# Performance work log

Hardware: AMD Instinct MI355X
Metric: run time of the kernel (lower is better)

## Reference

```python
import jax, jax.numpy as jnp
import numpy as np

T, B, I, H = 128, 256, 512, 1024  # time, batch, input_size, hidden_size


def setup_inputs() -> dict:
    key = jax.random.key(0)
    k1, k2, k3, k4, k5 = jax.random.split(key, 5)
    s = 1.0 / np.sqrt(H)  # matches torch GRUCell uniform(-1/sqrt(H), 1/sqrt(H)) scale
    return {
        "input_seq": jax.random.normal(k1, (T, B, I), dtype=jnp.float32),
        "W_ih": jax.random.uniform(k2, (3 * H, I), minval=-s, maxval=s, dtype=jnp.float32),
        "W_hh": jax.random.uniform(k3, (3 * H, H), minval=-s, maxval=s, dtype=jnp.float32),
        "b_ih": jax.random.uniform(k4, (3 * H,), minval=-s, maxval=s, dtype=jnp.float32),
        "b_hh": jax.random.uniform(k5, (3 * H,), minval=-s, maxval=s, dtype=jnp.float32),
    }


def reference(input_seq, W_ih, W_hh, b_ih, b_hh):
    # Original torch code calls GRUCell(input_seq[i]) with NO hidden state and never
    # feeds the output back, so hx = 0 at EVERY step -> no recurrence; fully vectorizable.
    Hd = W_hh.shape[1]
    # input gates for all timesteps at once: (T, B, 3H)
    gi = jnp.einsum('tbi,gi->tbg', input_seq, W_ih) + b_ih
    # hidden gates with hx = 0: zeros @ W_hh.T + b_hh == b_hh broadcast, shape (B, 3H)
    h0 = jnp.zeros((input_seq.shape[1], Hd), dtype=input_seq.dtype)
    gh = h0 @ W_hh.T + b_hh
    i_r, i_z, i_n = gi[..., :Hd], gi[..., Hd:2 * Hd], gi[..., 2 * Hd:]
    h_r, h_z, h_n = gh[..., :Hd], gh[..., Hd:2 * Hd], gh[..., 2 * Hd:]
    r = jax.nn.sigmoid(i_r + h_r)
    z = jax.nn.sigmoid(i_z + h_z)
    n = jnp.tanh(i_n + r * h_n)
    h = (1.0 - z) * n + z * h0  # z*h0 == 0, kept for faithfulness
    # torch.stack(output, dim=1) -> (B, T, H)
    return jnp.transpose(h, (1, 0, 2))
```

## Files before the change

### kernel.cpp

```cpp
#include <hip/hip_runtime.h>
#include <hip/hip_bf16.h>

using f32x4  = __attribute__((ext_vector_type(4))) float;
using bf16x8 = __attribute__((ext_vector_type(8))) short;
using s16x4  = __attribute__((ext_vector_type(4))) short;

#define TT 128
#define BB 256
#define II 512
#define HH 1024
#define MM (TT * BB)
#define BM 128
#define BH 64
#define BK 64
#define NTHREADS 256

__device__ __forceinline__ short f2bf(float f) {
    unsigned u = __float_as_uint(f);
    u = u + 0x7FFFu + ((u >> 16) & 1u);
    return (short)(u >> 16);
}

__device__ __forceinline__ float sigmoid_f(float x) {
    float e = __expf(-fabsf(x));
    float s = 1.0f / (1.0f + e);
    return x >= 0.0f ? s : 1.0f - s;
}

__device__ __forceinline__ float tanh_f(float x) {
    float e = __expf(-2.0f * fabsf(x));
    float t = (1.0f - e) / (1.0f + e);
    return x >= 0.0f ? t : -t;
}

__device__ __forceinline__ void gload_lds16(const void* g, void* l) {
    __builtin_amdgcn_global_load_lds((const __attribute__((address_space(1))) unsigned*)g,
                                     (__attribute__((address_space(3))) unsigned*)l,
                                     16, 0, 0);
}

__global__ __launch_bounds__(256)
void cvt_bf16_kernel(const float* __restrict__ src, short* __restrict__ dst, int n8) {
    const int stride = gridDim.x * blockDim.x;
    for (int i = blockIdx.x * blockDim.x + threadIdx.x; i < n8; i += stride) {
        f32x4 v0 = ((const f32x4*)src)[2 * i];
        f32x4 v1 = ((const f32x4*)src)[2 * i + 1];
        bf16x8 o;
        o[0] = f2bf(v0.x); o[1] = f2bf(v0.y); o[2] = f2bf(v0.z); o[3] = f2bf(v0.w);
        o[4] = f2bf(v1.x); o[5] = f2bf(v1.y); o[6] = f2bf(v1.z); o[7] = f2bf(v1.w);
        ((bf16x8*)dst)[i] = o;
    }
}

__global__ __launch_bounds__(NTHREADS, 3)
void gru_gemm_kernel(const short* __restrict__ Abf,
                     const short* __restrict__ Wbf,
                     const float* __restrict__ bih,
                     const float* __restrict__ bhh,
                     float* __restrict__ out)
{
    __shared__ short As[BM * BK];
    __shared__ short Ws[3 * BH * BK];

    const int tid  = threadIdx.x;
    const int wid  = tid >> 6;
    const int lane = tid & 63;
    const int l15  = lane & 15;
    const int l4   = lane >> 4;

    const int mtile = blockIdx.x >> 4;
    const int htile = blockIdx.x & 15;
    const int m0 = mtile * BM;
    const int h0 = htile * BH;

    const int lr8 = lane >> 3;
    const int lc  = lane & 7;
    const int csw = (lc * 16) ^ (lr8 << 4);

    f32x4 acc[2][12];
    #pragma unroll
    for (int i = 0; i < 2; ++i)
        #pragma unroll
        for (int j = 0; j < 12; ++j)
            acc[i][j] = (f32x4){0.f, 0.f, 0.f, 0.f};

    const char* Ab = (const char*)Abf;
    const char* Wb = (const char*)Wbf;

    for (int kt = 0; kt < II / BK; ++kt) {
        const int kb = kt * (BK * 2);

        #pragma unroll
        for (int j = 0; j < 4; ++j) {
            const int it  = wid * 4 + j;
            const int row = it * 8 + lr8;
            gload_lds16(Ab + (size_t)(m0 + row) * (II * 2) + kb + csw,
                        (char*)As + it * 1024);
        }
        #pragma unroll
        for (int j = 0; j < 6; ++j) {
            const int iw  = wid * 6 + j;
            const int row = iw * 8 + lr8;
            const int g   = row >> 6;
            const int wr  = row & 63;
            gload_lds16(Wb + (size_t)(g * HH + h0 + wr) * (II * 2) + kb + csw,
                        (char*)Ws + iw * 1024);
        }
        __syncthreads();

        const int xsw = (l15 & 7) << 4;
        #pragma unroll
        for (int kk = 0; kk < 2; ++kk) {
            const int cb = kk * 64 + l4 * 16;
            const int r0 = wid * 32 + l15;
            bf16x8 a0 = *(const bf16x8*)((const char*)As + r0 * 128 + (cb ^ xsw));
            bf16x8 a1 = *(const bf16x8*)((const char*)As + (r0 + 16) * 128 + (cb ^ xsw));
            #pragma unroll
            for (int nf = 0; nf < 12; ++nf) {
                const int rn = nf * 16 + l15;
                bf16x8 b = *(const bf16x8*)((const char*)Ws + rn * 128 + (cb ^ xsw));
                acc[0][nf] = __builtin_amdgcn_mfma_f32_16x16x32_bf16(a0, b, acc[0][nf], 0, 0, 0);
                acc[1][nf] = __builtin_amdgcn_mfma_f32_16x16x32_bf16(a1, b, acc[1][nf], 0, 0, 0);
            }
        }
        __syncthreads();
    }

    #pragma unroll
    for (int nf = 0; nf < 4; ++nf) {
        const int h = h0 + nf * 16 + l15;
        const float bir = bih[h]          + bhh[h];
        const float biz = bih[HH + h]     + bhh[HH + h];
        const float bin = bih[2 * HH + h];
        const float bhn = bhh[2 * HH + h];
        #pragma unroll
        for (int mf = 0; mf < 2; ++mf) {
            const f32x4 ra = acc[mf][nf];
            const f32x4 za = acc[mf][nf + 4];
            const f32x4 na = acc[mf][nf + 8];
            #pragma unroll
            for (int j = 0; j < 4; ++j) {
                const int m = m0 + wid * 32 + mf * 16 + l4 * 4 + j;
                const int t = m >> 8;
                const int b = m & 255;
                const float r = sigmoid_f(ra[j] + bir);
                const float z = sigmoid_f(za[j] + biz);
                const float n = tanh_f(na[j] + bin + r * bhn);
                out[(size_t)b * (TT * HH) + (size_t)t * HH + h] = (1.0f - z) * n;
            }
        }
    }
}

__global__ __launch_bounds__(NTHREADS, 2)
void gru_fused_kernel(const float* __restrict__ A,
                      const float* __restrict__ Wih,
                      const float* __restrict__ bih,
                      const float* __restrict__ bhh,
                      float* __restrict__ out)
{
    __shared__ short As[BM * BK];
    __shared__ short Ws[3 * BH * BK];

    const int tid  = threadIdx.x;
    const int wid  = tid >> 6;
    const int lane = tid & 63;
    const int l15  = lane & 15;
    const int l4   = lane >> 4;

    const int mtile = blockIdx.x >> 4;
    const int htile = blockIdx.x & 15;
    const int m0 = mtile * BM;
    const int h0 = htile * BH;

    const int rbase = tid >> 4;
    const int c4    = tid & 15;
    const int swz   = (rbase & 7) << 3;

    f32x4 acc[2][12];
    #pragma unroll
    for (int i = 0; i < 2; ++i)
        #pragma unroll
        for (int j = 0; j < 12; ++j)
            acc[i][j] = (f32x4){0.f, 0.f, 0.f, 0.f};

    for (int kt = 0; kt < II / BK; ++kt) {
        const int k0 = kt * BK;
        __syncthreads();
        const float* Ab = A + (size_t)(m0 + rbase) * II + k0 + c4 * 4;
        #pragma unroll
        for (int i = 0; i < 8; ++i) {
            f32x4 v = *(const f32x4*)(Ab + (size_t)i * 16 * II);
            s16x4 hv;
            hv.x = f2bf(v.x); hv.y = f2bf(v.y); hv.z = f2bf(v.z); hv.w = f2bf(v.w);
            const int idx = (i * 16 + rbase) * BK + ((c4 * 4) ^ swz);
            *(s16x4*)(As + idx) = hv;
        }
        #pragma unroll
        for (int i = 0; i < 12; ++i) {
            const int row = i * 16 + rbase;
            const int g   = row >> 6;
            const int r   = row & 63;
            f32x4 v = *(const f32x4*)(Wih + (size_t)(g * HH + h0 + r) * II + k0 + c4 * 4);
            s16x4 hv;
            hv.x = f2bf(v.x); hv.y = f2bf(v.y); hv.z = f2bf(v.z); hv.w = f2bf(v.w);
            const int idx = row * BK + ((c4 * 4) ^ swz);
            *(s16x4*)(Ws + idx) = hv;
        }
        __syncthreads();

        #pragma unroll
        for (int kk = 0; kk < 2; ++kk) {
            const int kc = kk * 32 + l4 * 8;
            const int r0 = wid * 32 + l15;
            const int r1 = r0 + 16;
            bf16x8 a0 = *(const bf16x8*)(As + r0 * BK + (kc ^ ((r0 & 7) << 3)));
            bf16x8 a1 = *(const bf16x8*)(As + r1 * BK + (kc ^ ((r1 & 7) << 3)));
            #pragma unroll
            for (int nf = 0; nf < 12; ++nf) {
                const int rn = nf * 16 + l15;
                bf16x8 b = *(const bf16x8*)(Ws + rn * BK + (kc ^ ((rn & 7) << 3)));
                acc[0][nf] = __builtin_amdgcn_mfma_f32_16x16x32_bf16(a0, b, acc[0][nf], 0, 0, 0);
                acc[1][nf] = __builtin_amdgcn_mfma_f32_16x16x32_bf16(a1, b, acc[1][nf], 0, 0, 0);
            }
        }
    }

    #pragma unroll
    for (int nf = 0; nf < 4; ++nf) {
        const int h = h0 + nf * 16 + l15;
        const float bir = bih[h]          + bhh[h];
        const float biz = bih[HH + h]     + bhh[HH + h];
        const float bin = bih[2 * HH + h];
        const float bhn = bhh[2 * HH + h];
        #pragma unroll
        for (int mf = 0; mf < 2; ++mf) {
            const f32x4 ra = acc[mf][nf];
            const f32x4 za = acc[mf][nf + 4];
            const f32x4 na = acc[mf][nf + 8];
            #pragma unroll
            for (int j = 0; j < 4; ++j) {
                const int m = m0 + wid * 32 + mf * 16 + l4 * 4 + j;
                const int t = m >> 8;
                const int b = m & 255;
                const float r = sigmoid_f(ra[j] + bir);
                const float z = sigmoid_f(za[j] + biz);
                const float n = tanh_f(na[j] + bin + r * bhn);
                out[(size_t)b * (TT * HH) + (size_t)t * HH + h] = (1.0f - z) * n;
            }
        }
    }
}

extern "C" void kernel_launch(void* const* d_in, const int* in_sizes, int n_in,
                              void* d_out, int out_size, void* d_ws, size_t ws_size,
                              hipStream_t stream) {
    const float* input = (const float*)d_in[0];
    const float* Wih   = (const float*)d_in[1];
    const float* bih   = (const float*)d_in[3];
    const float* bhh   = (const float*)d_in[4];
    float* out = (float*)d_out;

    const size_t nA = (size_t)MM * II;
    const size_t nW = (size_t)3 * HH * II;
    const size_t need = (nA + nW) * sizeof(short);

    const int nblocks = (MM / BM) * (HH / BH);

    if (ws_size >= need) {
        short* Abf = (short*)d_ws;
        short* Wbf = Abf + nA;
        cvt_bf16_kernel<<<2048, 256, 0, stream>>>(input, Abf, (int)(nA / 8));
        cvt_bf16_kernel<<<768,  256, 0, stream>>>(Wih,   Wbf, (int)(nW / 8));
        gru_gemm_kernel<<<nblocks, NTHREADS, 0, stream>>>(Abf, Wbf, bih, bhh, out);
    } else {
        gru_fused_kernel<<<nblocks, NTHREADS, 0, stream>>>(input, Wih, bih, bhh, out);
    }
}
```

Measured before the change: 318.6 us.

## Double-buffer LDS in 8-wave GEMM with larger M tile and merged conversion

Replaces the 4-wave 128x192 GEMM block with an 8-wave 256x192 block. It double-buffers the global-to-LDS loads across K steps, using explicit vmcnt waits and raw barriers so the next tile's loads overlap the current tile's MFMAs, and raises MFMA priority with setprio. The two fp32-to-bf16 conversion launches are merged into one kernel. The larger tile raises reuse of W from LDS and halves the block count. In exchange it uses about 112KB of LDS per block, which may limit occupancy, and depends on the hand-counted vmcnt value being correct.

```diff
diff --git a/kernel.cpp b/kernel.cpp
--- a/kernel.cpp
+++ b/kernel.cpp
@@ -10,10 +10,6 @@
 #define II 512
 #define HH 1024
 #define MM (TT * BB)
-#define BM 128
-#define BH 64
-#define BK 64
-#define NTHREADS 256
 
 __device__ __forceinline__ short f2bf(float f) {
     unsigned u = __float_as_uint(f);
@@ -40,11 +36,13 @@
 }
 
 __global__ __launch_bounds__(256)
-void cvt_bf16_kernel(const float* __restrict__ src, short* __restrict__ dst, int n8) {
+void cvt_both_kernel(const float* __restrict__ A, const float* __restrict__ W,
+                     short* __restrict__ dst, int nA8, int nTot8) {
     const int stride = gridDim.x * blockDim.x;
-    for (int i = blockIdx.x * blockDim.x + threadIdx.x; i < n8; i += stride) {
-        f32x4 v0 = ((const f32x4*)src)[2 * i];
-        f32x4 v1 = ((const f32x4*)src)[2 * i + 1];
+    for (int i = blockIdx.x * blockDim.x + threadIdx.x; i < nTot8; i += stride) {
+        const float* src = (i < nA8) ? (A + (size_t)i * 8) : (W + (size_t)(i - nA8) * 8);
+        f32x4 v0 = ((const f32x4*)src)[0];
+        f32x4 v1 = ((const f32x4*)src)[1];
         bf16x8 o;
         o[0] = f2bf(v0.x); o[1] = f2bf(v0.y); o[2] = f2bf(v0.z); o[3] = f2bf(v0.w);
         o[4] = f2bf(v1.x); o[5] = f2bf(v1.y); o[6] = f2bf(v1.z); o[7] = f2bf(v1.w);
@@ -52,115 +50,154 @@
     }
 }
 
-__global__ __launch_bounds__(NTHREADS, 3)
-void gru_gemm_kernel(const short* __restrict__ Abf,
-                     const short* __restrict__ Wbf,
-                     const float* __restrict__ bih,
-                     const float* __restrict__ bhh,
-                     float* __restrict__ out)
+__global__ __launch_bounds__(512, 2)
+void gru_gemm8_kernel(const short* __restrict__ Abf,
+                      const short* __restrict__ Wbf,
+                      const float* __restrict__ bih,
+                      const float* __restrict__ bhh,
+                      float* __restrict__ out)
 {
-    __shared__ short As[BM * BK];
-    __shared__ short Ws[3 * BH * BK];
+    __shared__ char lds[114688];
 
     const int tid  = threadIdx.x;
     const int wid  = tid >> 6;
     const int lane = tid & 63;
     const int l15  = lane & 15;
     const int l4   = lane >> 4;
+    const int wm   = wid >> 1;
+    const int wn   = wid & 1;
 
     const int mtile = blockIdx.x >> 4;
     const int htile = blockIdx.x & 15;
-    const int m0 = mtile * BM;
-    const int h0 = htile * BH;
+    const int m0 = mtile * 256;
+    const int h0 = htile * 64;
 
     const int lr8 = lane >> 3;
     const int lc  = lane & 7;
     const int csw = (lc * 16) ^ (lr8 << 4);
 
-    f32x4 acc[2][12];
-    #pragma unroll
-    for (int i = 0; i < 2; ++i)
-        #pragma unroll
-        for (int j = 0; j < 12; ++j)
-            acc[i][j] = (f32x4){0.f, 0.f, 0.f, 0.f};
-
     const char* Ab = (const char*)Abf;
     const char* Wb = (const char*)Wbf;
 
-    for (int kt = 0; kt < II / BK; ++kt) {
-        const int kb = kt * (BK * 2);
-
-        #pragma unroll
-        for (int j = 0; j < 4; ++j) {
-            const int it  = wid * 4 + j;
-            const int row = it * 8 + lr8;
-            gload_lds16(Ab + (size_t)(m0 + row) * (II * 2) + kb + csw,
-                        (char*)As + it * 1024);
-        }
-        #pragma unroll
-        for (int j = 0; j < 6; ++j) {
-            const int iw  = wid * 6 + j;
-            const int row = iw * 8 + lr8;
-            const int g   = row >> 6;
-            const int wr  = row & 63;
-            gload_lds16(Wb + (size_t)(g * HH + h0 + wr) * (II * 2) + kb + csw,
-                        (char*)Ws + iw * 1024);
-        }
-        __syncthreads();
-
-        const int xsw = (l15 & 7) << 4;
+    size_t aAddr[4];
+    size_t wAddr[3];
+    #pragma unroll
+    for (int j = 0; j < 4; ++j)
+        aAddr[j] = (size_t)(m0 + (wid * 4 + j) * 8 + lr8) * 1024 + csw;
+    #pragma unroll
+    for (int j = 0; j < 3; ++j) {
+        const int row = (wid * 3 + j) * 8 + lr8;
+        const int g   = row >> 6;
+        const int wr  = row & 63;
+        wAddr[j] = (size_t)(g * HH + h0 + wr) * 1024 + csw;
+    }
+
+    f32x4 acc[4][3][2];
+    #pragma unroll
+    for (int mf = 0; mf < 4; ++mf)
+        #pragma unroll
+        for (int g = 0; g < 3; ++g)
+            #pragma unroll
+            for (int nf = 0; nf < 2; ++nf)
+                acc[mf][g][nf] = (f32x4){0.f, 0.f, 0.f, 0.f};
+
+    #define STAGE(t, p)                                                          \
+        do {                                                                     \
+            const int kb_ = (t) * 128;                                           \
+            _Pragma("unroll")                                                    \
+            for (int j = 0; j < 4; ++j)                                          \
+                gload_lds16(Ab + aAddr[j] + kb_,                                 \
+                            lds + (p) * 32768 + (wid * 4 + j) * 1024);           \
+            _Pragma("unroll")                                                    \
+            for (int j = 0; j < 3; ++j)                                          \
+                gload_lds16(Wb + wAddr[j] + kb_,                                 \
+                            lds + 65536 + (p) * 24576 + (wid * 3 + j) * 1024);   \
+        } while (0)
+
+    STAGE(0, 0);
+
+    const int xsw = (l15 & 7) << 4;
+
+    for (int t = 0; t < 8; ++t) {
+        const int p = t & 1;
+        if (t < 7) {
+            STAGE(t + 1, p ^ 1);
+            asm volatile("s_waitcnt vmcnt(7)" ::: "memory");
+        } else {
+            asm volatile("s_waitcnt vmcnt(0)" ::: "memory");
+        }
+        __builtin_amdgcn_s_barrier();
+
+        const char* Abase = lds + p * 32768;
+        const char* Wbase = lds + 65536 + p * 24576;
+
         #pragma unroll
         for (int kk = 0; kk < 2; ++kk) {
             const int cb = kk * 64 + l4 * 16;
-            const int r0 = wid * 32 + l15;
-            bf16x8 a0 = *(const bf16x8*)((const char*)As + r0 * 128 + (cb ^ xsw));
-            bf16x8 a1 = *(const bf16x8*)((const char*)As + (r0 + 16) * 128 + (cb ^ xsw));
-            #pragma unroll
-            for (int nf = 0; nf < 12; ++nf) {
-                const int rn = nf * 16 + l15;
-                bf16x8 b = *(const bf16x8*)((const char*)Ws + rn * 128 + (cb ^ xsw));
-                acc[0][nf] = __builtin_amdgcn_mfma_f32_16x16x32_bf16(a0, b, acc[0][nf], 0, 0, 0);
-                acc[1][nf] = __builtin_amdgcn_mfma_f32_16x16x32_bf16(a1, b, acc[1][nf], 0, 0, 0);
+            bf16x8 a[4], b[3][2];
+            #pragma unroll
+            for (int mf = 0; mf < 4; ++mf) {
+                const int r = wm * 64 + mf * 16 + l15;
+                a[mf] = *(const bf16x8*)(Abase + r * 128 + (cb ^ xsw));
             }
-        }
-        __syncthreads();
-    }
-
-    #pragma unroll
-    for (int nf = 0; nf < 4; ++nf) {
-        const int h = h0 + nf * 16 + l15;
+            #pragma unroll
+            for (int g = 0; g < 3; ++g)
+                #pragma unroll
+                for (int nf = 0; nf < 2; ++nf) {
+                    const int rn = g * 64 + wn * 32 + nf * 16 + l15;
+                    b[g][nf] = *(const bf16x8*)(Wbase + rn * 128 + (cb ^ xsw));
+                }
+            __builtin_amdgcn_s_setprio(1);
+            #pragma unroll
+            for (int mf = 0; mf < 4; ++mf)
+                #pragma unroll
+                for (int g = 0; g < 3; ++g)
+                    #pragma unroll
+                    for (int nf = 0; nf < 2; ++nf)
+                        acc[mf][g][nf] = __builtin_amdgcn_mfma_f32_16x16x32_bf16(
+                            a[mf], b[g][nf], acc[mf][g][nf], 0, 0, 0);
+            __builtin_amdgcn_s_setprio(0);
+        }
+        asm volatile("" ::: "memory");
+        __builtin_amdgcn_s_barrier();
+    }
+    #undef STAGE
+
+    #pragma unroll
+    for (int nf = 0; nf < 2; ++nf) {
+        const int h = h0 + wn * 32 + nf * 16 + l15;
         const float bir = bih[h]          + bhh[h];
         const float biz = bih[HH + h]     + bhh[HH + h];
         const float bin = bih[2 * HH + h];
         const float bhn = bhh[2 * HH + h];
         #pragma unroll
-        for (int mf = 0; mf < 2; ++mf) {
-            const f32x4 ra = acc[mf][nf];
-            const f32x4 za = acc[mf][nf + 4];
-            const f32x4 na = acc[mf][nf + 8];
+        for (int mf = 0; mf < 4; ++mf) {
+            const f32x4 ra = acc[mf][0][nf];
+            const f32x4 za = acc[mf][1][nf];
+            const f32x4 na = acc[mf][2][nf];
             #pragma unroll
             for (int j = 0; j < 4; ++j) {
-                const int m = m0 + wid * 32 + mf * 16 + l4 * 4 + j;
-                const int t = m >> 8;
-                const int b = m & 255;
+                const int m = m0 + wm * 64 + mf * 16 + l4 * 4 + j;
+                const int tt = m >> 8;
+                const int bb = m & 255;
                 const float r = sigmoid_f(ra[j] + bir);
                 const float z = sigmoid_f(za[j] + biz);
                 const float n = tanh_f(na[j] + bin + r * bhn);
-                out[(size_t)b * (TT * HH) + (size_t)t * HH + h] = (1.0f - z) * n;
+                out[(size_t)bb * (TT * HH) + (size_t)tt * HH + h] = (1.0f - z) * n;
             }
         }
     }
 }
 
-__global__ __launch_bounds__(NTHREADS, 2)
+__global__ __launch_bounds__(256, 2)
 void gru_fused_kernel(const float* __restrict__ A,
                       const float* __restrict__ Wih,
                       const float* __restrict__ bih,
                       const float* __restrict__ bhh,
                       float* __restrict__ out)
 {
-    __shared__ short As[BM * BK];
-    __shared__ short Ws[3 * BH * BK];
+    __shared__ short As[128 * 64];
+    __shared__ short Ws[192 * 64];
 
     const int tid  = threadIdx.x;
     const int wid  = tid >> 6;
@@ -170,8 +207,8 @@
 
     const int mtile = blockIdx.x >> 4;
     const int htile = blockIdx.x & 15;
-    const int m0 = mtile * BM;
-    const int h0 = htile * BH;
+    const int m0 = mtile * 128;
+    const int h0 = htile * 64;
 
     const int rbase = tid >> 4;
     const int c4    = tid & 15;
@@ -184,8 +221,8 @@
         for (int j = 0; j < 12; ++j)
             acc[i][j] = (f32x4){0.f, 0.f, 0.f, 0.f};
 
-    for (int kt = 0; kt < II / BK; ++kt) {
-        const int k0 = kt * BK;
+    for (int kt = 0; kt < II / 64; ++kt) {
+        const int k0 = kt * 64;
         __syncthreads();
         const float* Ab = A + (size_t)(m0 + rbase) * II + k0 + c4 * 4;
         #pragma unroll
@@ -193,8 +230,7 @@
             f32x4 v = *(const f32x4*)(Ab + (size_t)i * 16 * II);
             s16x4 hv;
             hv.x = f2bf(v.x); hv.y = f2bf(v.y); hv.z = f2bf(v.z); hv.w = f2bf(v.w);
-            const int idx = (i * 16 + rbase) * BK + ((c4 * 4) ^ swz);
-            *(s16x4*)(As + idx) = hv;
+            *(s16x4*)(As + (i * 16 + rbase) * 64 + ((c4 * 4) ^ swz)) = hv;
         }
         #pragma unroll
         for (int i = 0; i < 12; ++i) {
@@ -204,8 +240,7 @@
             f32x4 v = *(const f32x4*)(Wih + (size_t)(g * HH + h0 + r) * II + k0 + c4 * 4);
             s16x4 hv;
             hv.x = f2bf(v.x); hv.y = f2bf(v.y); hv.z = f2bf(v.z); hv.w = f2bf(v.w);
-            const int idx = row * BK + ((c4 * 4) ^ swz);
-            *(s16x4*)(Ws + idx) = hv;
+            *(s16x4*)(Ws + row * 64 + ((c4 * 4) ^ swz)) = hv;
         }
         __syncthreads();
 
@@ -213,13 +248,12 @@
         for (int kk = 0; kk < 2; ++kk) {
             const int kc = kk * 32 + l4 * 8;
             const int r0 = wid * 32 + l15;
-            const int r1 = r0 + 16;
-            bf16x8 a0 = *(const bf16x8*)(As + r0 * BK + (kc ^ ((r0 & 7) << 3)));
-            bf16x8 a1 = *(const bf16x8*)(As + r1 * BK + (kc ^ ((r1 & 7) << 3)));
+            bf16x8 a0 = *(const bf16x8*)(As + r0 * 64 + (kc ^ ((r0 & 7) << 3)));
+            bf16x8 a1 = *(const bf16x8*)(As + (r0 + 16) * 64 + (kc ^ ((r0 & 7) << 3)));
             #pragma unroll
             for (int nf = 0; nf < 12; ++nf) {
                 const int rn = nf * 16 + l15;
-                bf16x8 b = *(const bf16x8*)(Ws + rn * BK + (kc ^ ((rn & 7) << 3)));
+                bf16x8 b = *(const bf16x8*)(Ws + rn * 64 + (kc ^ ((rn & 7) << 3)));
                 acc[0][nf] = __builtin_amdgcn_mfma_f32_16x16x32_bf16(a0, b, acc[0][nf], 0, 0, 0);
                 acc[1][nf] = __builtin_amdgcn_mfma_f32_16x16x32_bf16(a1, b, acc[1][nf], 0, 0, 0);
             }
@@ -241,12 +275,12 @@
             #pragma unroll
             for (int j = 0; j < 4; ++j) {
                 const int m = m0 + wid * 32 + mf * 16 + l4 * 4 + j;
-                const int t = m >> 8;
-                const int b = m & 255;
+                const int tt = m >> 8;
+                const int bb = m & 255;
                 const float r = sigmoid_f(ra[j] + bir);
                 const float z = sigmoid_f(za[j] + biz);
                 const float n = tanh_f(na[j] + bin + r * bhn);
-                out[(size_t)b * (TT * HH) + (size_t)t * HH + h] = (1.0f - z) * n;
+                out[(size_t)bb * (TT * HH) + (size_t)tt * HH + h] = (1.0f - z) * n;
             }
         }
     }
@@ -265,15 +299,14 @@
     const size_t nW = (size_t)3 * HH * II;
     const size_t need = (nA + nW) * sizeof(short);
 
-    const int nblocks = (MM / BM) * (HH / BH);
-
     if (ws_size >= need) {
         short* Abf = (short*)d_ws;
-        short* Wbf = Abf + nA;
-        cvt_bf16_kernel<<<2048, 256, 0, stream>>>(input, Abf, (int)(nA / 8));
-        cvt_bf16_kernel<<<768,  256, 0, stream>>>(Wih,   Wbf, (int)(nW / 8));
-        gru_gemm_kernel<<<nblocks, NTHREADS, 0, stream>>>(Abf, Wbf, bih, bhh, out);
+        cvt_both_kernel<<<4096, 256, 0, stream>>>(input, Wih, Abf,
+                                                  (int)(nA / 8), (int)((nA + nW) / 8));
+        const int nblocks = (MM / 256) * (HH / 64);
+        gru_gemm8_kernel<<<nblocks, 512, 0, stream>>>(Abf, Abf + nA, bih, bhh, out);
     } else {
-        gru_fused_kernel<<<nblocks, NTHREADS, 0, stream>>>(input, Wih, bih, bhh, out);
-    }
-}
+        const int nblocks = (MM / 128) * (HH / 64);
+        gru_fused_kernel<<<nblocks, 256, 0, stream>>>(input, Wih, bih, bhh, out);
+    }
+}
```

Result: slower. 341.2 us (+7.1%).
